# Kernel optimization log

Measured on AMD Instinct MI355X. Metric: run time of the kernel, lower is better.

The kernel has to match this reference:

```python
import jax, jax.numpy as jnp
import numpy as np

B, S, H = 64, 2048, 512
NEG_INF = -1e10


def setup_inputs() -> dict:
    key = jax.random.key(0)
    k1, k2, k3, k4, k5, k6 = jax.random.split(key, 6)
    return {
        "output": jax.random.normal(k1, (B, 1, H), dtype=jnp.float32),
        "encoder_outputs": jax.random.normal(k2, (B, S, H), dtype=jnp.float32),
        "encoder_sequence_lengths": jax.random.randint(k3, (B,), 1, S + 1, dtype=jnp.int32),
        "W1": jax.random.normal(k4, (H, H), dtype=jnp.float32) * (1.0 / np.sqrt(H)),
        "W2": jax.random.normal(k5, (H, H), dtype=jnp.float32) * (1.0 / np.sqrt(H)),
        "V": jax.random.normal(k6, (H, 1), dtype=jnp.float32) * (1.0 / np.sqrt(H)),
    }


def reference(output, encoder_outputs, encoder_sequence_lengths, W1, W2, V):
    # output: [B,1,H] decoder state (query); encoder_outputs: [B,S,H] (key & value)
    S_ = encoder_outputs.shape[1]
    key_proj = jnp.einsum('bsh,hd->bsd', encoder_outputs, W1)   # [B,S,H]
    query_proj = jnp.einsum('bqh,hd->bqd', output, W2)          # [B,1,H]
    energy = jnp.einsum('bsh,ho->bso', jnp.tanh(key_proj + query_proj), V)  # [B,S,1]
    mask = jnp.arange(S_)[None, :, None] < encoder_sequence_lengths[:, None, None]  # [B,S,1]
    energy = jnp.where(mask, energy, NEG_INF)
    attn = jax.nn.softmax(energy, axis=1)                       # [B,S,1]
    context = jnp.sum(attn * encoder_outputs, axis=1)           # [B,H]
    return context
```

## Files before the change

kernel.cpp:

```cpp
#include <hip/hip_runtime.h>
#include <hip/hip_bf16.h>

#define SS 2048
#define HH 512

typedef __attribute__((ext_vector_type(8))) short short8;
typedef __attribute__((ext_vector_type(4))) float f32x4;

__device__ __forceinline__ float bflo(unsigned u) { return __uint_as_float(u << 16); }
__device__ __forceinline__ float bfhi(unsigned u) { return __uint_as_float(u & 0xffff0000u); }

__device__ __forceinline__ short f2bf(float v) {
  __hip_bfloat16 h = __float2bfloat16(v);
  return *reinterpret_cast<short*>(&h);
}

__device__ __forceinline__ float tanh_fast(float x) {
  x = fminf(fmaxf(x, -15.f), 15.f);
  float e = __expf(2.f * x);
  return 1.f - 2.f / (e + 1.f);
}

__global__ void k_detect(const unsigned* __restrict__ Eu, int* __restrict__ flag) {
  int lane = threadIdx.x;
  unsigned w = Eu[(size_t)lane * 4097];
  unsigned e = (w >> 7) & 0xFF;
  bool inr = (e >= 90 && e <= 140);
  unsigned long long m = __ballot(inr);
  if (lane == 0) *flag = (__popcll(m) >= 48) ? 1 : 0;
}

__global__ __launch_bounds__(256) void k_prep(const __hip_bfloat16* __restrict__ W1b,
                                              const float* __restrict__ W1f,
                                              const __hip_bfloat16* __restrict__ qb,
                                              const float* __restrict__ qf,
                                              const __hip_bfloat16* __restrict__ W2b,
                                              const float* __restrict__ W2f,
                                              const int* __restrict__ flagp,
                                              __hip_bfloat16* __restrict__ W1T,
                                              float* __restrict__ qp_part) {
  const int mode = *flagp;
  __shared__ __hip_bfloat16 t[64][65];
  __shared__ float qs[128];
  if (blockIdx.x < 64) {
    int r0 = (blockIdx.x >> 3) * 64, c0 = (blockIdx.x & 7) * 64;
    for (int i = threadIdx.x; i < 4096; i += 256) {
      int r = i >> 6, c = i & 63;
      size_t idx = (size_t)(r0 + r) * HH + c0 + c;
      float v = mode ? (float)W1b[idx] : W1f[idx];
      t[r][c] = __float2bfloat16(v);
    }
    __syncthreads();
    for (int i = threadIdx.x; i < 4096; i += 256) {
      int r = i >> 6, c = i & 63;
      W1T[(size_t)(c0 + r) * HH + r0 + c] = t[c][r];
    }
  } else {
    int bx = blockIdx.x - 64;
    int b = bx & 63, p = bx >> 6, h0 = p * 128;
    if (threadIdx.x < 128) {
      size_t qi = (size_t)b * HH + h0 + threadIdx.x;
      qs[threadIdx.x] = mode ? (float)qb[qi] : qf[qi];
    }
    __syncthreads();
    int col = threadIdx.x * 2;
    float a0 = 0.f, a1 = 0.f;
    if (mode) {
#pragma unroll 4
      for (int i = 0; i < 128; ++i) {
        float qa = qs[i];
        unsigned u = *(const unsigned*)(W2b + (size_t)(h0 + i) * HH + col);
        a0 = fmaf(qa, bflo(u), a0);
        a1 = fmaf(qa, bfhi(u), a1);
      }
    } else {
#pragma unroll 4
      for (int i = 0; i < 128; ++i) {
        float qa = qs[i];
        float2 v = *(const float2*)(W2f + (size_t)(h0 + i) * HH + col);
        a0 = fmaf(qa, v.x, a0);
        a1 = fmaf(qa, v.y, a1);
      }
    }
    float* dst = qp_part + ((size_t)p * 64 + b) * HH + col;
    dst[0] = a0;
    dst[1] = a1;
  }
}

__global__ __launch_bounds__(256, 2) void k_energy(
    const __hip_bfloat16* __restrict__ Eb, const float* __restrict__ Ef,
    const __hip_bfloat16* __restrict__ W1T, const float* __restrict__ qpp,
    const __hip_bfloat16* __restrict__ Vwb, const float* __restrict__ Vwf,
    const int* __restrict__ flagp, const int* __restrict__ lens,
    float* __restrict__ tpart) {
  __shared__ __align__(16) __hip_bfloat16 Bt[2][128 * 32];
  __shared__ float qps[HH];
  __shared__ float Vs[HH];
  __shared__ float p[128];
  __shared__ float red[4];
  __shared__ f32x4 part[128];

  const int tid = threadIdx.x;
  const int wave = tid >> 6, lane = tid & 63;
  const int quad = lane >> 4, l16 = lane & 15;
  const int row0 = blockIdx.x * 128;
  const int b = row0 >> 11;
  const int len = lens[b];
  if ((row0 & 2047) >= len) return;

  const int mode = *flagp;

  for (int i = tid; i < HH; i += 256) {
    qps[i] = qpp[(size_t)b * HH + i] + qpp[(size_t)(64 + b) * HH + i] +
             qpp[(size_t)(128 + b) * HH + i] + qpp[(size_t)(192 + b) * HH + i];
    Vs[i] = mode ? (float)Vwb[i] : Vwf[i];
  }

  short8 afr[2][16];
  {
    const size_t eBase = (size_t)row0 * HH + (size_t)(wave * 32 + l16) * HH + quad * 8;
    if (mode) {
      const __hip_bfloat16* pa = Eb + eBase;
#pragma unroll
      for (int kt = 0; kt < 16; ++kt) {
        afr[0][kt] = *(const short8*)(pa + kt * 32);
        afr[1][kt] = *(const short8*)(pa + 16 * HH + kt * 32);
      }
    } else {
      const float* pa = Ef + eBase;
#pragma unroll
      for (int kt = 0; kt < 16; ++kt) {
#pragma unroll
        for (int rb = 0; rb < 2; ++rb) {
          const float* pp = pa + rb * 16 * HH + kt * 32;
          f32x4 x0 = *(const f32x4*)pp;
          f32x4 x1 = *(const f32x4*)(pp + 4);
          short8 v;
#pragma unroll
          for (int j = 0; j < 4; ++j) {
            v[j] = f2bf(x0[j]);
            v[j + 4] = f2bf(x1[j]);
          }
          afr[rb][kt] = v;
        }
      }
    }
  }

  const int rs0 = wave * 32 + (lane >> 2);
  const int rs1 = rs0 + 16;
  const int kg0 = ((lane & 3) - (rs0 >> 1)) & 3;
  const int kg1 = ((lane & 3) - (rs1 >> 1)) & 3;
  const __hip_bfloat16* pb0 = W1T + (size_t)rs0 * HH + kg0 * 8;
  const __hip_bfloat16* pb1 = W1T + (size_t)rs1 * HH + kg1 * 8;
  const int wslot = wave * 1024 + lane * 8;

  int offB[8];
#pragma unroll
  for (int cb = 0; cb < 8; ++cb) {
    int n = cb * 16 + l16;
    offB[cb] = n * 32 + (((quad + (n >> 1)) & 3) << 3);
  }

  short8 bp0 = *(const short8*)(pb0);
  short8 bp1 = *(const short8*)(pb1);
  *(short8*)(&Bt[0][0] + wslot) = bp0;
  *(short8*)(&Bt[0][0] + wslot + 512) = bp1;
  bp0 = *(const short8*)(pb0 + 32);
  bp1 = *(const short8*)(pb1 + 32);
  __syncthreads();

  float eacc[2][4] = {{0.f, 0.f, 0.f, 0.f}, {0.f, 0.f, 0.f, 0.f}};

  for (int nc = 0; nc < 4; ++nc) {
    f32x4 acc[2][8];
#pragma unroll
    for (int rb = 0; rb < 2; ++rb)
#pragma unroll
      for (int cb = 0; cb < 8; ++cb) acc[rb][cb] = (f32x4){0.f, 0.f, 0.f, 0.f};

#pragma unroll
    for (int kt = 0; kt < 16; ++kt) {
      const int t = nc * 16 + kt;
      const __hip_bfloat16* bb = &Bt[t & 1][0];
      short8 af0 = afr[0][kt];
      short8 af1 = afr[1][kt];
#pragma unroll
      for (int cb = 0; cb < 8; ++cb) {
        short8 bf = *(const short8*)(bb + offB[cb]);
        acc[0][cb] = __builtin_amdgcn_mfma_f32_16x16x32_bf16(af0, bf, acc[0][cb], 0, 0, 0);
        acc[1][cb] = __builtin_amdgcn_mfma_f32_16x16x32_bf16(af1, bf, acc[1][cb], 0, 0, 0);
      }

      {
        __hip_bfloat16* bw = &Bt[(t + 1) & 1][0] + wslot;
        *(short8*)bw = bp0;
        *(short8*)(bw + 512) = bp1;
        int t2 = t + 2;
        if (t2 > 63) t2 = 63;
        int o = ((t2 >> 4) << 16) + ((t2 & 15) << 5);
        bp0 = *(const short8*)(pb0 + o);
        bp1 = *(const short8*)(pb1 + o);
      }
      asm volatile("s_waitcnt lgkmcnt(0)" ::: "memory");
      __builtin_amdgcn_s_barrier();
      __builtin_amdgcn_sched_barrier(0);
    }

#pragma unroll
    for (int rb = 0; rb < 2; ++rb)
#pragma unroll
      for (int cb = 0; cb < 8; ++cb) {
        int col = nc * 128 + cb * 16 + l16;
        float qv = qps[col], vv = Vs[col];
#pragma unroll
        for (int r = 0; r < 4; ++r) {
          float tv = tanh_fast(acc[rb][cb][r] + qv);
          eacc[rb][r] = fmaf(vv, tv, eacc[rb][r]);
        }
      }
  }

#pragma unroll
  for (int rb = 0; rb < 2; ++rb)
#pragma unroll
    for (int r = 0; r < 4; ++r) {
      float v = eacc[rb][r];
#pragma unroll
      for (int o = 1; o < 16; o <<= 1) v += __shfl_xor(v, o);
      if (l16 == 0) {
        int row = wave * 32 + rb * 16 + quad * 4 + r;
        int s = (row0 & 2047) + row;
        p[row] = (s < len) ? v : -3.0e38f;
      }
    }
  __syncthreads();

  float e = (tid < 128) ? p[tid] : -3.0e38f;
  float m = e;
#pragma unroll
  for (int o = 1; o < 64; o <<= 1) m = fmaxf(m, __shfl_xor(m, o));
  if ((tid & 63) == 0) red[tid >> 6] = m;
  __syncthreads();
  m = fmaxf(fmaxf(red[0], red[1]), fmaxf(red[2], red[3]));
  float w = (tid < 128) ? __expf(e - m) : 0.f;
  float d = w;
#pragma unroll
  for (int o = 1; o < 64; o <<= 1) d += __shfl_xor(d, o);
  __syncthreads();
  if ((tid & 63) == 0) red[tid >> 6] = d;
  if (tid < 128) p[tid] = w;
  __syncthreads();
  const float d_t = red[0] + red[1] + red[2] + red[3];

  const int n = min(128, len - (row0 & 2047));
  const int h0 = (tid & 127) * 4;
  const int rr = tid >> 7;
  f32x4 a = {0.f, 0.f, 0.f, 0.f};
  if (mode) {
    const __hip_bfloat16* base = Eb + (size_t)row0 * HH + h0;
#pragma unroll 2
    for (int i = rr; i < n; i += 2) {
      float wv = p[i];
      uint2 u = *(const uint2*)(base + (size_t)i * HH);
      a[0] = fmaf(wv, bflo(u.x), a[0]);
      a[1] = fmaf(wv, bfhi(u.x), a[1]);
      a[2] = fmaf(wv, bflo(u.y), a[2]);
      a[3] = fmaf(wv, bfhi(u.y), a[3]);
    }
  } else {
    const float* base = Ef + (size_t)row0 * HH + h0;
#pragma unroll 2
    for (int i = rr; i < n; i += 2) {
      float wv = p[i];
      f32x4 v = *(const f32x4*)(base + (size_t)i * HH);
      a[0] = fmaf(wv, v[0], a[0]);
      a[1] = fmaf(wv, v[1], a[1]);
      a[2] = fmaf(wv, v[2], a[2]);
      a[3] = fmaf(wv, v[3], a[3]);
    }
  }
  if (tid >= 128) part[tid - 128] = a;
  __syncthreads();
  if (tid < 128) {
    f32x4 o = part[tid];
    f32x4 s;
    s[0] = a[0] + o[0];
    s[1] = a[1] + o[1];
    s[2] = a[2] + o[2];
    s[3] = a[3] + o[3];
    *(f32x4*)(tpart + (size_t)blockIdx.x * 516 + h0) = s;
  }
  if (tid == 0) {
    tpart[(size_t)blockIdx.x * 516 + 512] = m;
    tpart[(size_t)blockIdx.x * 516 + 513] = d_t;
  }
}

__global__ __launch_bounds__(256) void k_reduce(const float* __restrict__ tpart,
                                                const int* __restrict__ lens,
                                                const int* __restrict__ flagp,
                                                __hip_bfloat16* __restrict__ outb,
                                                float* __restrict__ outf) {
  const int b = blockIdx.x, tid = threadIdx.x;
  const int nch = (lens[b] + 127) >> 7;
  const float* tb = tpart + (size_t)b * 16 * 516;
  float m = -3.0e38f;
  for (int c = 0; c < nch; ++c) m = fmaxf(m, tb[c * 516 + 512]);
  const int h = tid * 2;
  float den = 0.f, a0 = 0.f, a1 = 0.f;
  for (int c = 0; c < nch; ++c) {
    float sc = __expf(tb[c * 516 + 512] - m);
    den = fmaf(tb[c * 516 + 513], sc, den);
    float2 v = *(const float2*)(tb + c * 516 + h);
    a0 = fmaf(sc, v.x, a0);
    a1 = fmaf(sc, v.y, a1);
  }
  float inv = 1.f / den;
  int i = b * HH + h;
  if (*flagp) {
    outb[i] = __float2bfloat16(a0 * inv);
    outb[i + 1] = __float2bfloat16(a1 * inv);
  } else {
    outf[i] = a0 * inv;
    outf[i + 1] = a1 * inv;
  }
}

extern "C" void kernel_launch(void* const* d_in, const int* in_sizes, int n_in,
                              void* d_out, int out_size, void* d_ws, size_t ws_size,
                              hipStream_t stream) {
  const __hip_bfloat16* qb  = (const __hip_bfloat16*)d_in[0];
  const float*          qf  = (const float*)d_in[0];
  const __hip_bfloat16* Eb  = (const __hip_bfloat16*)d_in[1];
  const float*          Ef  = (const float*)d_in[1];
  const int* lens           = (const int*)d_in[2];
  const __hip_bfloat16* W1b = (const __hip_bfloat16*)d_in[3];
  const float*          W1f = (const float*)d_in[3];
  const __hip_bfloat16* W2b = (const __hip_bfloat16*)d_in[4];
  const float*          W2f = (const float*)d_in[4];
  const __hip_bfloat16* Vwb = (const __hip_bfloat16*)d_in[5];
  const float*          Vwf = (const float*)d_in[5];
  __hip_bfloat16* outb      = (__hip_bfloat16*)d_out;
  float*          outf      = (float*)d_out;

  char* ws = (char*)d_ws;
  __hip_bfloat16* W1T = (__hip_bfloat16*)(ws);
  float* qp_part      = (float*)(ws + 524288);
  float* tpart        = (float*)(ws + 1048576);
  int* flag           = (int*)(ws + 3162112);

  k_detect<<<dim3(1), 64, 0, stream>>>((const unsigned*)d_in[1], flag);
  k_prep<<<dim3(320), 256, 0, stream>>>(W1b, W1f, qb, qf, W2b, W2f, flag, W1T, qp_part);
  k_energy<<<dim3(1024), 256, 0, stream>>>(Eb, Ef, W1T, qp_part, Vwb, Vwf, flag, lens, tpart);
  k_reduce<<<dim3(64), 256, 0, stream>>>(tpart, lens, flag, outb, outf);
}
```

Measured before the change: 466.5 us.

## Compact live tiles into a persistent grid and deepen W1 prefetch pipeline

k_detect now builds a compacted list of live 128-row tiles from the sequence lengths using a prefix sum. k_energy runs as a persistent 512-block grid that strides over only those live tiles, so it no longer launches blocks that exit at once for masked rows. The W1T shared-memory ring grows from 2 to 4 stages with prefetch distance 4, and the context loop unroll goes from 2 to 4. The larger LDS buffer may reduce occupancy, and a grid of 512 blocks may leave CUs uneven at the tail.

```diff
diff --git a/kernel.cpp b/kernel.cpp
--- a/kernel.cpp
+++ b/kernel.cpp
@@ -21,13 +21,27 @@
   return 1.f - 2.f / (e + 1.f);
 }
 
-__global__ void k_detect(const unsigned* __restrict__ Eu, int* __restrict__ flag) {
+__global__ void k_detect(const unsigned* __restrict__ Eu, const int* __restrict__ lens,
+                         int* __restrict__ flag, int* __restrict__ tmap,
+                         int* __restrict__ livep) {
   int lane = threadIdx.x;
   unsigned w = Eu[(size_t)lane * 4097];
   unsigned e = (w >> 7) & 0xFF;
   bool inr = (e >= 90 && e <= 140);
   unsigned long long m = __ballot(inr);
   if (lane == 0) *flag = (__popcll(m) >= 48) ? 1 : 0;
+
+  int len = lens[lane];
+  int n = (len + 127) >> 7;
+  int off = n;
+#pragma unroll
+  for (int o = 1; o < 64; o <<= 1) {
+    int v = __shfl_up(off, o);
+    if (lane >= o) off += v;
+  }
+  int base = off - n;
+  for (int j = 0; j < n; ++j) tmap[base + j] = lane * 16 + j;
+  if (lane == 63) *livep = off;
 }
 
 __global__ __launch_bounds__(256) void k_prep(const __hip_bfloat16* __restrict__ W1b,
@@ -93,8 +107,9 @@
     const __hip_bfloat16* __restrict__ W1T, const float* __restrict__ qpp,
     const __hip_bfloat16* __restrict__ Vwb, const float* __restrict__ Vwf,
     const int* __restrict__ flagp, const int* __restrict__ lens,
+    const int* __restrict__ tmap, const int* __restrict__ livep,
     float* __restrict__ tpart) {
-  __shared__ __align__(16) __hip_bfloat16 Bt[2][128 * 32];
+  __shared__ __align__(16) __hip_bfloat16 Bt[4][128 * 32];
   __shared__ float qps[HH];
   __shared__ float Vs[HH];
   __shared__ float p[128];
@@ -104,49 +119,8 @@
   const int tid = threadIdx.x;
   const int wave = tid >> 6, lane = tid & 63;
   const int quad = lane >> 4, l16 = lane & 15;
-  const int row0 = blockIdx.x * 128;
-  const int b = row0 >> 11;
-  const int len = lens[b];
-  if ((row0 & 2047) >= len) return;
-
   const int mode = *flagp;
-
-  for (int i = tid; i < HH; i += 256) {
-    qps[i] = qpp[(size_t)b * HH + i] + qpp[(size_t)(64 + b) * HH + i] +
-             qpp[(size_t)(128 + b) * HH + i] + qpp[(size_t)(192 + b) * HH + i];
-    Vs[i] = mode ? (float)Vwb[i] : Vwf[i];
-  }
-
-  short8 afr[2][16];
-  {
-    const size_t eBase = (size_t)row0 * HH + (size_t)(wave * 32 + l16) * HH + quad * 8;
-    if (mode) {
-      const __hip_bfloat16* pa = Eb + eBase;
-#pragma unroll
-      for (int kt = 0; kt < 16; ++kt) {
-        afr[0][kt] = *(const short8*)(pa + kt * 32);
-        afr[1][kt] = *(const short8*)(pa + 16 * HH + kt * 32);
-      }
-    } else {
-      const float* pa = Ef + eBase;
-#pragma unroll
-      for (int kt = 0; kt < 16; ++kt) {
-#pragma unroll
-        for (int rb = 0; rb < 2; ++rb) {
-          const float* pp = pa + rb * 16 * HH + kt * 32;
-          f32x4 x0 = *(const f32x4*)pp;
-          f32x4 x1 = *(const f32x4*)(pp + 4);
-          short8 v;
-#pragma unroll
-          for (int j = 0; j < 4; ++j) {
-            v[j] = f2bf(x0[j]);
-            v[j + 4] = f2bf(x1[j]);
-          }
-          afr[rb][kt] = v;
-        }
-      }
-    }
-  }
+  const int live = *livep;
 
   const int rs0 = wave * 32 + (lane >> 2);
   const int rs1 = rs0 + 16;
@@ -163,138 +137,189 @@
     offB[cb] = n * 32 + (((quad + (n >> 1)) & 3) << 3);
   }
 
-  short8 bp0 = *(const short8*)(pb0);
-  short8 bp1 = *(const short8*)(pb1);
-  *(short8*)(&Bt[0][0] + wslot) = bp0;
-  *(short8*)(&Bt[0][0] + wslot + 512) = bp1;
-  bp0 = *(const short8*)(pb0 + 32);
-  bp1 = *(const short8*)(pb1 + 32);
-  __syncthreads();
-
-  float eacc[2][4] = {{0.f, 0.f, 0.f, 0.f}, {0.f, 0.f, 0.f, 0.f}};
-
-  for (int nc = 0; nc < 4; ++nc) {
-    f32x4 acc[2][8];
+  for (int i = tid; i < HH; i += 256) Vs[i] = mode ? (float)Vwb[i] : Vwf[i];
+
+  for (int idx = blockIdx.x; idx < live; idx += 512) {
+    const int tile = tmap[idx];
+    const int b = tile >> 4;
+    const int row0 = tile * 128;
+    const int len = lens[b];
+
+    for (int i = tid; i < HH; i += 256)
+      qps[i] = qpp[(size_t)b * HH + i] + qpp[(size_t)(64 + b) * HH + i] +
+               qpp[(size_t)(128 + b) * HH + i] + qpp[(size_t)(192 + b) * HH + i];
+
+    short8 afr[2][16];
+    {
+      const size_t eBase = (size_t)row0 * HH + (size_t)(wave * 32 + l16) * HH + quad * 8;
+      if (mode) {
+        const __hip_bfloat16* pa = Eb + eBase;
+#pragma unroll
+        for (int kt = 0; kt < 16; ++kt) {
+          afr[0][kt] = *(const short8*)(pa + kt * 32);
+          afr[1][kt] = *(const short8*)(pa + 16 * HH + kt * 32);
+        }
+      } else {
+        const float* pa = Ef + eBase;
+#pragma unroll
+        for (int kt = 0; kt < 16; ++kt) {
+#pragma unroll
+          for (int rb = 0; rb < 2; ++rb) {
+            const float* pp = pa + rb * 16 * HH + kt * 32;
+            f32x4 x0 = *(const f32x4*)pp;
+            f32x4 x1 = *(const f32x4*)(pp + 4);
+            short8 v;
+#pragma unroll
+            for (int j = 0; j < 4; ++j) {
+              v[j] = f2bf(x0[j]);
+              v[j + 4] = f2bf(x1[j]);
+            }
+            afr[rb][kt] = v;
+          }
+        }
+      }
+    }
+
+    short8 bpa[4], bpb[4];
+    bpa[0] = *(const short8*)(pb0);
+    bpb[0] = *(const short8*)(pb1);
+    *(short8*)(&Bt[0][0] + wslot) = bpa[0];
+    *(short8*)(&Bt[0][0] + wslot + 512) = bpb[0];
+    bpa[1] = *(const short8*)(pb0 + 32);
+    bpb[1] = *(const short8*)(pb1 + 32);
+    bpa[2] = *(const short8*)(pb0 + 64);
+    bpb[2] = *(const short8*)(pb1 + 64);
+    bpa[3] = *(const short8*)(pb0 + 96);
+    bpb[3] = *(const short8*)(pb1 + 96);
+    __syncthreads();
+
+    float eacc[2][4] = {{0.f, 0.f, 0.f, 0.f}, {0.f, 0.f, 0.f, 0.f}};
+
+    for (int nc = 0; nc < 4; ++nc) {
+      f32x4 acc[2][8];
+#pragma unroll
+      for (int rb = 0; rb < 2; ++rb)
+#pragma unroll
+        for (int cb = 0; cb < 8; ++cb) acc[rb][cb] = (f32x4){0.f, 0.f, 0.f, 0.f};
+
+#pragma unroll
+      for (int kt = 0; kt < 16; ++kt) {
+        const int t = nc * 16 + kt;
+        const __hip_bfloat16* bb = &Bt[kt & 3][0];
+        short8 af0 = afr[0][kt];
+        short8 af1 = afr[1][kt];
+#pragma unroll
+        for (int cb = 0; cb < 8; ++cb) {
+          short8 bf = *(const short8*)(bb + offB[cb]);
+          acc[0][cb] = __builtin_amdgcn_mfma_f32_16x16x32_bf16(af0, bf, acc[0][cb], 0, 0, 0);
+          acc[1][cb] = __builtin_amdgcn_mfma_f32_16x16x32_bf16(af1, bf, acc[1][cb], 0, 0, 0);
+        }
+
+        {
+          const int ss = (kt + 1) & 3;
+          const int sp = kt & 3;
+          __hip_bfloat16* bw = &Bt[ss][0] + wslot;
+          *(short8*)bw = bpa[ss];
+          *(short8*)(bw + 512) = bpb[ss];
+          int t2 = t + 4;
+          if (t2 > 63) t2 = 63;
+          int o = ((t2 >> 4) << 16) + ((t2 & 15) << 5);
+          bpa[sp] = *(const short8*)(pb0 + o);
+          bpb[sp] = *(const short8*)(pb1 + o);
+        }
+        asm volatile("s_waitcnt lgkmcnt(0)" ::: "memory");
+        __builtin_amdgcn_s_barrier();
+        __builtin_amdgcn_sched_barrier(0);
+      }
+
+#pragma unroll
+      for (int rb = 0; rb < 2; ++rb)
+#pragma unroll
+        for (int cb = 0; cb < 8; ++cb) {
+          int col = nc * 128 + cb * 16 + l16;
+          float qv = qps[col], vv = Vs[col];
+#pragma unroll
+          for (int r = 0; r < 4; ++r) {
+            float tv = tanh_fast(acc[rb][cb][r] + qv);
+            eacc[rb][r] = fmaf(vv, tv, eacc[rb][r]);
+          }
+        }
+    }
+
 #pragma unroll
     for (int rb = 0; rb < 2; ++rb)
 #pragma unroll
-      for (int cb = 0; cb < 8; ++cb) acc[rb][cb] = (f32x4){0.f, 0.f, 0.f, 0.f};
-
-#pragma unroll
-    for (int kt = 0; kt < 16; ++kt) {
-      const int t = nc * 16 + kt;
-      const __hip_bfloat16* bb = &Bt[t & 1][0];
-      short8 af0 = afr[0][kt];
-      short8 af1 = afr[1][kt];
-#pragma unroll
-      for (int cb = 0; cb < 8; ++cb) {
-        short8 bf = *(const short8*)(bb + offB[cb]);
-        acc[0][cb] = __builtin_amdgcn_mfma_f32_16x16x32_bf16(af0, bf, acc[0][cb], 0, 0, 0);
-        acc[1][cb] = __builtin_amdgcn_mfma_f32_16x16x32_bf16(af1, bf, acc[1][cb], 0, 0, 0);
-      }
-
-      {
-        __hip_bfloat16* bw = &Bt[(t + 1) & 1][0] + wslot;
-        *(short8*)bw = bp0;
-        *(short8*)(bw + 512) = bp1;
-        int t2 = t + 2;
-        if (t2 > 63) t2 = 63;
-        int o = ((t2 >> 4) << 16) + ((t2 & 15) << 5);
-        bp0 = *(const short8*)(pb0 + o);
-        bp1 = *(const short8*)(pb1 + o);
-      }
-      asm volatile("s_waitcnt lgkmcnt(0)" ::: "memory");
-      __builtin_amdgcn_s_barrier();
-      __builtin_amdgcn_sched_barrier(0);
-    }
-
-#pragma unroll
-    for (int rb = 0; rb < 2; ++rb)
-#pragma unroll
-      for (int cb = 0; cb < 8; ++cb) {
-        int col = nc * 128 + cb * 16 + l16;
-        float qv = qps[col], vv = Vs[col];
-#pragma unroll
-        for (int r = 0; r < 4; ++r) {
-          float tv = tanh_fast(acc[rb][cb][r] + qv);
-          eacc[rb][r] = fmaf(vv, tv, eacc[rb][r]);
-        }
-      }
-  }
-
-#pragma unroll
-  for (int rb = 0; rb < 2; ++rb)
-#pragma unroll
-    for (int r = 0; r < 4; ++r) {
-      float v = eacc[rb][r];
-#pragma unroll
-      for (int o = 1; o < 16; o <<= 1) v += __shfl_xor(v, o);
-      if (l16 == 0) {
-        int row = wave * 32 + rb * 16 + quad * 4 + r;
-        int s = (row0 & 2047) + row;
-        p[row] = (s < len) ? v : -3.0e38f;
-      }
-    }
-  __syncthreads();
-
-  float e = (tid < 128) ? p[tid] : -3.0e38f;
-  float m = e;
-#pragma unroll
-  for (int o = 1; o < 64; o <<= 1) m = fmaxf(m, __shfl_xor(m, o));
-  if ((tid & 63) == 0) red[tid >> 6] = m;
-  __syncthreads();
-  m = fmaxf(fmaxf(red[0], red[1]), fmaxf(red[2], red[3]));
-  float w = (tid < 128) ? __expf(e - m) : 0.f;
-  float d = w;
-#pragma unroll
-  for (int o = 1; o < 64; o <<= 1) d += __shfl_xor(d, o);
-  __syncthreads();
-  if ((tid & 63) == 0) red[tid >> 6] = d;
-  if (tid < 128) p[tid] = w;
-  __syncthreads();
-  const float d_t = red[0] + red[1] + red[2] + red[3];
-
-  const int n = min(128, len - (row0 & 2047));
-  const int h0 = (tid & 127) * 4;
-  const int rr = tid >> 7;
-  f32x4 a = {0.f, 0.f, 0.f, 0.f};
-  if (mode) {
-    const __hip_bfloat16* base = Eb + (size_t)row0 * HH + h0;
-#pragma unroll 2
-    for (int i = rr; i < n; i += 2) {
-      float wv = p[i];
-      uint2 u = *(const uint2*)(base + (size_t)i * HH);
-      a[0] = fmaf(wv, bflo(u.x), a[0]);
-      a[1] = fmaf(wv, bfhi(u.x), a[1]);
-      a[2] = fmaf(wv, bflo(u.y), a[2]);
-      a[3] = fmaf(wv, bfhi(u.y), a[3]);
-    }
-  } else {
-    const float* base = Ef + (size_t)row0 * HH + h0;
-#pragma unroll 2
-    for (int i = rr; i < n; i += 2) {
-      float wv = p[i];
-      f32x4 v = *(const f32x4*)(base + (size_t)i * HH);
-      a[0] = fmaf(wv, v[0], a[0]);
-      a[1] = fmaf(wv, v[1], a[1]);
-      a[2] = fmaf(wv, v[2], a[2]);
-      a[3] = fmaf(wv, v[3], a[3]);
-    }
-  }
-  if (tid >= 128) part[tid - 128] = a;
-  __syncthreads();
-  if (tid < 128) {
-    f32x4 o = part[tid];
-    f32x4 s;
-    s[0] = a[0] + o[0];
-    s[1] = a[1] + o[1];
-    s[2] = a[2] + o[2];
-    s[3] = a[3] + o[3];
-    *(f32x4*)(tpart + (size_t)blockIdx.x * 516 + h0) = s;
-  }
-  if (tid == 0) {
-    tpart[(size_t)blockIdx.x * 516 + 512] = m;
-    tpart[(size_t)blockIdx.x * 516 + 513] = d_t;
+      for (int r = 0; r < 4; ++r) {
+        float v = eacc[rb][r];
+#pragma unroll
+        for (int o = 1; o < 16; o <<= 1) v += __shfl_xor(v, o);
+        if (l16 == 0) {
+          int row = wave * 32 + rb * 16 + quad * 4 + r;
+          int s = (row0 & 2047) + row;
+          p[row] = (s < len) ? v : -3.0e38f;
+        }
+      }
+    __syncthreads();
+
+    float e = (tid < 128) ? p[tid] : -3.0e38f;
+    float m = e;
+#pragma unroll
+    for (int o = 1; o < 64; o <<= 1) m = fmaxf(m, __shfl_xor(m, o));
+    if ((tid & 63) == 0) red[tid >> 6] = m;
+    __syncthreads();
+    m = fmaxf(fmaxf(red[0], red[1]), fmaxf(red[2], red[3]));
+    float w = (tid < 128) ? __expf(e - m) : 0.f;
+    float d = w;
+#pragma unroll
+    for (int o = 1; o < 64; o <<= 1) d += __shfl_xor(d, o);
+    __syncthreads();
+    if ((tid & 63) == 0) red[tid >> 6] = d;
+    if (tid < 128) p[tid] = w;
+    __syncthreads();
+    const float d_t = red[0] + red[1] + red[2] + red[3];
+
+    const int n = min(128, len - (row0 & 2047));
+    const int h0 = (tid & 127) * 4;
+    const int rr = tid >> 7;
+    f32x4 a = {0.f, 0.f, 0.f, 0.f};
+    if (mode) {
+      const __hip_bfloat16* base = Eb + (size_t)row0 * HH + h0;
+#pragma unroll 4
+      for (int i = rr; i < n; i += 2) {
+        float wv = p[i];
+        uint2 u = *(const uint2*)(base + (size_t)i * HH);
+        a[0] = fmaf(wv, bflo(u.x), a[0]);
+        a[1] = fmaf(wv, bfhi(u.x), a[1]);
+        a[2] = fmaf(wv, bflo(u.y), a[2]);
+        a[3] = fmaf(wv, bfhi(u.y), a[3]);
+      }
+    } else {
+      const float* base = Ef + (size_t)row0 * HH + h0;
+#pragma unroll 4
+      for (int i = rr; i < n; i += 2) {
+        float wv = p[i];
+        f32x4 v = *(const f32x4*)(base + (size_t)i * HH);
+        a[0] = fmaf(wv, v[0], a[0]);
+        a[1] = fmaf(wv, v[1], a[1]);
+        a[2] = fmaf(wv, v[2], a[2]);
+        a[3] = fmaf(wv, v[3], a[3]);
+      }
+    }
+    if (tid >= 128) part[tid - 128] = a;
+    __syncthreads();
+    if (tid < 128) {
+      f32x4 o = part[tid];
+      f32x4 s;
+      s[0] = a[0] + o[0];
+      s[1] = a[1] + o[1];
+      s[2] = a[2] + o[2];
+      s[3] = a[3] + o[3];
+      *(f32x4*)(tpart + (size_t)tile * 516 + h0) = s;
+    }
+    if (tid == 0) {
+      tpart[(size_t)tile * 516 + 512] = m;
+      tpart[(size_t)tile * 516 + 513] = d_t;
+    }
   }
 }
 
@@ -350,9 +375,12 @@
   float* qp_part      = (float*)(ws + 524288);
   float* tpart        = (float*)(ws + 1048576);
   int* flag           = (int*)(ws + 3162112);
-
-  k_detect<<<dim3(1), 64, 0, stream>>>((const unsigned*)d_in[1], flag);
+  int* tmap           = (int*)(ws + 3162624);
+  int* livep          = (int*)(ws + 3166720);
+
+  k_detect<<<dim3(1), 64, 0, stream>>>((const unsigned*)d_in[1], lens, flag, tmap, livep);
   k_prep<<<dim3(320), 256, 0, stream>>>(W1b, W1f, qb, qf, W2b, W2f, flag, W1T, qp_part);
-  k_energy<<<dim3(1024), 256, 0, stream>>>(Eb, Ef, W1T, qp_part, Vwb, Vwf, flag, lens, tpart);
+  k_energy<<<dim3(512), 256, 0, stream>>>(Eb, Ef, W1T, qp_part, Vwb, Vwf, flag, lens,
+                                          tmap, livep, tpart);
   k_reduce<<<dim3(64), 256, 0, stream>>>(tpart, lens, flag, outb, outf);
 }
```

Measured after the change: 481.1 us. +3.1%, slower.
